# Optimization experiments

Measured on AMD Instinct MI355X. Metric: run time of the kernel, lower is better.

## Reference

```python
import jax, jax.numpy as jnp
import numpy as np

B, T, C, H = 4, 2048, 1024, 16
D = C // H  # head dim = 64

def setup_inputs() -> dict:
    key = jax.random.key(0)
    k1, k2, k3 = jax.random.split(key, 3)
    y = jax.random.normal(k1, (B, T, C), dtype=jnp.float32)
    W_attn = jax.random.normal(k2, (C, 3 * C), dtype=jnp.float32) * (1.0 / np.sqrt(C))
    b_attn = jnp.zeros((3 * C,), dtype=jnp.float32)
    W_proj = jax.random.normal(k3, (C, C), dtype=jnp.float32) * (1.0 / np.sqrt(C))
    b_proj = jnp.zeros((C,), dtype=jnp.float32)
    return {"y": y, "W_attn": W_attn, "b_attn": b_attn, "W_proj": W_proj, "b_proj": b_proj}

def reference(y, W_attn, b_attn, W_proj, b_proj):
    # qkv projection: [B,T,C] @ [C,3C] -> split into q,k,v
    qkv = y @ W_attn + b_attn
    q, k, v = jnp.split(qkv, 3, axis=-1)
    # [B,T,C] -> [B,H,T,D]
    q = q.reshape(B, T, H, D).swapaxes(1, 2)
    k = k.reshape(B, T, H, D).swapaxes(1, 2)
    v = v.reshape(B, T, H, D).swapaxes(1, 2)
    # scaled dot-product attention, non-causal (config default), dropout=0
    att = jnp.einsum('bhtd,bhrd->bhtr', q, k) * (1.0 / jnp.sqrt(jnp.float32(D)))
    att = jax.nn.softmax(att, axis=-1)
    out = jnp.einsum('bhts,bhsd->bhtd', att, v)
    out = out.swapaxes(1, 2).reshape(B, T, C)
    return out @ W_proj + b_proj
```

## Files before the change

kernel.cpp:

```cpp
#include <hip/hip_runtime.h>
#include <hip/hip_bf16.h>
#include <stdint.h>

#define B_ 4
#define T_ 2048
#define C_ 1024
#define H_ 16
#define D_ 64

typedef short bf16x8 __attribute__((ext_vector_type(8)));
typedef float f32x4 __attribute__((ext_vector_type(4)));
typedef unsigned short u16;

#define QSCALE 0.18033688011112042f

__device__ __forceinline__ u16 f2bf(float f) {
    __hip_bfloat16 h = __float2bfloat16(f);
    return *reinterpret_cast<u16*>(&h);
}

__device__ __forceinline__ float fexp2(float x) {
    float r;
    asm("v_exp_f32 %0, %1" : "=v"(r) : "v"(x));
    return r;
}

__device__ __forceinline__ void gload16(const void* g, void* l) {
    __builtin_amdgcn_global_load_lds(
        (const __attribute__((address_space(1))) unsigned int*)g,
        (__attribute__((address_space(3))) unsigned int*)l, 16, 0, 0);
}

__global__ void k_cast_bf16(const float* __restrict__ src, u16* __restrict__ dst, int n) {
    int i = (blockIdx.x * blockDim.x + threadIdx.x) * 4;
    if (i >= n) return;
    float4 f = *reinterpret_cast<const float4*>(src + i);
    ushort4 o;
    o.x = f2bf(f.x); o.y = f2bf(f.y); o.z = f2bf(f.z); o.w = f2bf(f.w);
    *reinterpret_cast<ushort4*>(dst + i) = o;
}

__global__ void k_transpose_bf16(const float* __restrict__ src, u16* __restrict__ dst,
                                 int R, int Cc) {
    __shared__ float tile[32][33];
    int c0 = blockIdx.x * 32, r0 = blockIdx.y * 32;
    int tx = threadIdx.x, ty = threadIdx.y;
#pragma unroll
    for (int i = 0; i < 4; i++)
        tile[ty + i * 8][tx] = src[(size_t)(r0 + ty + i * 8) * Cc + c0 + tx];
    __syncthreads();
#pragma unroll
    for (int i = 0; i < 4; i++)
        dst[(size_t)(c0 + ty + i * 8) * R + r0 + tx] = f2bf(tile[tx][ty + i * 8]);
}

template <int EPI>
__launch_bounds__(256, 2)
__global__ void k_gemm(const u16* __restrict__ A, const u16* __restrict__ Bt,
                       const float* __restrict__ bias, int K, int N,
                       float* __restrict__ outf,
                       u16* __restrict__ qw, u16* __restrict__ kw, u16* __restrict__ vw) {
    __shared__ u16 As[128 * 64];
    __shared__ u16 Bs[128 * 64];
    const int tid = threadIdx.x;
    const int lane = tid & 63, w = tid >> 6;
    const int m0 = blockIdx.x * 128, n0 = blockIdx.y * 128;
    const int wm = (w >> 1) * 64, wn = (w & 1) * 64;
    const int lr = lane & 15, lg = lane >> 4;

    f32x4 acc[4][4];
#pragma unroll
    for (int i = 0; i < 4; i++)
#pragma unroll
        for (int j = 0; j < 4; j++) acc[i][j] = (f32x4){0.f, 0.f, 0.f, 0.f};

    const int nk = K >> 6;
    for (int kt = 0; kt < nk; ++kt) {
        const int k0 = kt * 64;
#pragma unroll
        for (int i = 0; i < 4; i++) {
            int c = i * 256 + tid;
            int row = c >> 3, k8 = (c & 7) << 3;
            gload16(A + (size_t)(m0 + row) * K + k0 + k8, (char*)As + i * 4096 + w * 1024);
            gload16(Bt + (size_t)(n0 + row) * K + k0 + k8, (char*)Bs + i * 4096 + w * 1024);
        }
        __syncthreads();
#pragma unroll
        for (int kk = 0; kk < 2; ++kk) {
            bf16x8 af[4], bfr[4];
#pragma unroll
            for (int mf = 0; mf < 4; ++mf)
                af[mf] = *reinterpret_cast<const bf16x8*>(&As[(wm + mf * 16 + lr) * 64 + kk * 32 + lg * 8]);
#pragma unroll
            for (int nf = 0; nf < 4; ++nf)
                bfr[nf] = *reinterpret_cast<const bf16x8*>(&Bs[(wn + nf * 16 + lr) * 64 + kk * 32 + lg * 8]);
#pragma unroll
            for (int mf = 0; mf < 4; ++mf)
#pragma unroll
                for (int nf = 0; nf < 4; ++nf)
                    acc[mf][nf] = __builtin_amdgcn_mfma_f32_16x16x32_bf16(af[mf], bfr[nf], acc[mf][nf], 0, 0, 0);
        }
        __syncthreads();
    }

    if (EPI == 0) {
#pragma unroll
        for (int mf = 0; mf < 4; ++mf)
#pragma unroll
            for (int nf = 0; nf < 4; ++nf) {
                int ng = n0 + wn + nf * 16 + lr;
                float bs = bias[ng];
#pragma unroll
                for (int r = 0; r < 4; ++r) {
                    int mg = m0 + wm + mf * 16 + lg * 4 + r;
                    outf[(size_t)mg * N + ng] = acc[mf][nf][r] + bs;
                }
            }
    } else {
        const int sec = n0 >> 10;
        const float sc = (sec == 0) ? QSCALE : 1.0f;
#pragma unroll
        for (int mf = 0; mf < 4; ++mf)
#pragma unroll
            for (int nf = 0; nf < 4; ++nf) {
                int ng = n0 + wn + nf * 16 + lr;
                float bs = bias[ng];
                int hd = ng & 1023;
                int h = hd >> 6, d = hd & 63;
                int mgb = m0 + wm + mf * 16 + lg * 4;
                int b = mgb >> 11, t0v = mgb & 2047;
                if (sec == 2) {
                    ushort4 pk;
                    pk.x = f2bf(acc[mf][nf][0] + bs);
                    pk.y = f2bf(acc[mf][nf][1] + bs);
                    pk.z = f2bf(acc[mf][nf][2] + bs);
                    pk.w = f2bf(acc[mf][nf][3] + bs);
                    *reinterpret_cast<ushort4*>(&vw[((size_t)(b * H_ + h) * D_ + d) * T_ + t0v]) = pk;
                } else {
                    u16* dst = (sec == 0) ? qw : kw;
#pragma unroll
                    for (int r = 0; r < 4; ++r)
                        dst[((size_t)(b * H_ + h) * T_ + t0v + r) * D_ + d] = f2bf((acc[mf][nf][r] + bs) * sc);
                }
            }
    }
}

__launch_bounds__(256, 4)
__global__ void k_attn(const u16* __restrict__ qw, const u16* __restrict__ kw,
                       const u16* __restrict__ vw, u16* __restrict__ attn) {
    __shared__ u16 Ks[2][64][64];
    __shared__ u16 Vs[2][64][64];
    const int tid = threadIdx.x, lane = tid & 63, w = tid >> 6;
    const int lr = lane & 15, lg = lane >> 4;
    const int bid = blockIdx.x;
    const int logical = (bid & 7) * 128 + (bid >> 3);
    const int bh = logical >> 4, qb = logical & 15;
    const int b = bh >> 4, h = bh & 15;
    const int q0 = qb * 128 + w * 32;
    const u16* qbase = qw + (size_t)bh * T_ * D_;
    const u16* kbase = kw + (size_t)bh * T_ * D_;
    const u16* vbase = vw + (size_t)bh * D_ * T_;

    bf16x8 qf[2][2];
#pragma unroll
    for (int jq = 0; jq < 2; jq++)
#pragma unroll
        for (int kd = 0; kd < 2; kd++)
            qf[jq][kd] = *reinterpret_cast<const bf16x8*>(
                &qbase[(size_t)(q0 + jq * 16 + lr) * D_ + kd * 32 + lg * 8]);

    auto stageK = [&](int kt, int buf) {
#pragma unroll
        for (int i = 0; i < 2; i++) {
            int idx = i * 256 + tid;
            int row = idx >> 3, ch = idx & 7;
            int gch = ch ^ ((row & 3) | (((row >> 3) & 1) << 2));
            gload16(kbase + ((size_t)(kt * 64 + row) * 64 + gch * 8),
                    (char*)&Ks[buf][0][0] + i * 4096 + w * 1024);
        }
    };
    auto stageV = [&](int kt, int buf) {
#pragma unroll
        for (int i = 0; i < 2; i++) {
            int idx = i * 256 + tid;
            int row = idx >> 3, ch = idx & 7;
            int gch = ch ^ (row & 7);
            gload16(vbase + ((size_t)row * T_ + kt * 64 + gch * 8),
                    (char*)&Vs[buf][0][0] + i * 4096 + w * 1024);
        }
    };

    f32x4 o[4][2];
#pragma unroll
    for (int md = 0; md < 4; md++)
#pragma unroll
        for (int jq = 0; jq < 2; jq++) o[md][jq] = (f32x4){0.f, 0.f, 0.f, 0.f};
    float l_run[2] = {0.f, 0.f};

    const int karow_base = ((lr >> 2) << 3) + (lr & 3);
    const int skl = ((lr & 3) | (((lr >> 2) & 1) << 2)) << 4;

    const int NT = T_ / 64;
    stageK(0, 0);
    stageV(0, 0);

    for (int kt = 0; kt < NT; ++kt) {
        const int cur = kt & 1;
        if (kt + 1 < NT) {
            stageK(kt + 1, cur ^ 1);
            stageV(kt + 1, cur ^ 1);
            asm volatile("s_waitcnt vmcnt(4)" ::: "memory");
        } else {
            asm volatile("s_waitcnt vmcnt(0)" ::: "memory");
        }
        __builtin_amdgcn_s_barrier();

        bf16x8 pfrag[2][2];
#pragma unroll
        for (int g = 0; g < 2; g++) {
            f32x4 st[2][2];
#pragma unroll
            for (int t = 0; t < 2; t++)
#pragma unroll
                for (int jq = 0; jq < 2; jq++) st[t][jq] = (f32x4){0.f, 0.f, 0.f, 0.f};
            __builtin_amdgcn_s_setprio(1);
#pragma unroll
            for (int t = 0; t < 2; t++) {
                int row = g * 32 + karow_base + t * 4;
#pragma unroll
                for (int kd = 0; kd < 2; kd++) {
                    bf16x8 ka = *reinterpret_cast<const bf16x8*>(
                        (const char*)&Ks[cur][0][0] + row * 128 + ((kd * 64 + lg * 16) ^ skl));
#pragma unroll
                    for (int jq = 0; jq < 2; jq++)
                        st[t][jq] = __builtin_amdgcn_mfma_f32_16x16x32_bf16(ka, qf[jq][kd], st[t][jq], 0, 0, 0);
                }
            }
            __builtin_amdgcn_s_setprio(0);
#pragma unroll
            for (int jq = 0; jq < 2; jq++) {
                float p0 = fexp2(st[0][jq][0]), p1 = fexp2(st[0][jq][1]);
                float p2 = fexp2(st[0][jq][2]), p3 = fexp2(st[0][jq][3]);
                float p4 = fexp2(st[1][jq][0]), p5 = fexp2(st[1][jq][1]);
                float p6 = fexp2(st[1][jq][2]), p7 = fexp2(st[1][jq][3]);
                l_run[jq] += ((p0 + p1) + (p2 + p3)) + ((p4 + p5) + (p6 + p7));
                pfrag[jq][g] = (bf16x8){(short)f2bf(p0), (short)f2bf(p1),
                                        (short)f2bf(p2), (short)f2bf(p3),
                                        (short)f2bf(p4), (short)f2bf(p5),
                                        (short)f2bf(p6), (short)f2bf(p7)};
            }
        }

#pragma unroll
        for (int g = 0; g < 2; g++) {
            bf16x8 va[4];
#pragma unroll
            for (int md = 0; md < 4; md++) {
                int row = md * 16 + lr;
                va[md] = *reinterpret_cast<const bf16x8*>(
                    (const char*)&Vs[cur][0][0] + row * 128 + ((g * 64 + lg * 16) ^ ((row & 7) << 4)));
            }
            __builtin_amdgcn_s_setprio(1);
#pragma unroll
            for (int md = 0; md < 4; md++)
#pragma unroll
                for (int jq = 0; jq < 2; jq++)
                    o[md][jq] = __builtin_amdgcn_mfma_f32_16x16x32_bf16(va[md], pfrag[jq][g], o[md][jq], 0, 0, 0);
            __builtin_amdgcn_s_setprio(0);
        }

        __builtin_amdgcn_s_barrier();
    }

#pragma unroll
    for (int jq = 0; jq < 2; jq++) {
        float l = l_run[jq];
        l += __shfl_xor(l, 16);
        l += __shfl_xor(l, 32);
        float rinv = 1.f / l;
        int q = q0 + jq * 16 + lr;
#pragma unroll
        for (int md = 0; md < 4; md++) {
            int d0 = md * 16 + lg * 4;
            ushort4 pk;
            pk.x = f2bf(o[md][jq][0] * rinv);
            pk.y = f2bf(o[md][jq][1] * rinv);
            pk.z = f2bf(o[md][jq][2] * rinv);
            pk.w = f2bf(o[md][jq][3] * rinv);
            *reinterpret_cast<ushort4*>(&attn[((size_t)(b * T_ + q)) * C_ + h * D_ + d0]) = pk;
        }
    }
}

extern "C" void kernel_launch(void* const* d_in, const int* in_sizes, int n_in,
                              void* d_out, int out_size, void* d_ws, size_t ws_size,
                              hipStream_t stream) {
    const float* y = (const float*)d_in[0];
    const float* W_attn = (const float*)d_in[1];
    const float* b_attn = (const float*)d_in[2];
    const float* W_proj = (const float*)d_in[3];
    const float* b_proj = (const float*)d_in[4];

    char* ws = (char*)d_ws;
    u16* y_bf = (u16*)(ws);
    u16* WaT  = (u16*)(ws + 16777216);
    u16* WpT  = (u16*)(ws + 16777216 + 6291456);
    u16* q_ws = (u16*)(ws + 25165824);
    u16* k_ws = (u16*)(ws + 25165824 + 16777216);
    u16* v_ws = (u16*)(ws + 25165824 + 33554432);
    u16* attn = (u16*)(ws + 25165824 + 50331648);

    k_cast_bf16<<<8192, 256, 0, stream>>>(y, y_bf, B_ * T_ * C_);
    k_transpose_bf16<<<dim3(96, 32), dim3(32, 8), 0, stream>>>(W_attn, WaT, 1024, 3072);
    k_transpose_bf16<<<dim3(32, 32), dim3(32, 8), 0, stream>>>(W_proj, WpT, 1024, 1024);
    k_gemm<1><<<dim3(64, 24), 256, 0, stream>>>(y_bf, WaT, b_attn, 1024, 3072,
                                                nullptr, q_ws, k_ws, v_ws);
    k_attn<<<1024, 256, 0, stream>>>(q_ws, k_ws, v_ws, attn);
    k_gemm<0><<<dim3(64, 8), 256, 0, stream>>>(attn, WpT, b_proj, 1024, 1024,
                                               (float*)d_out, nullptr, nullptr, nullptr);
}
```

Baseline: 200.1 us.

## Fuse prep kernels into one launch and widen attention waves to 64 queries

The three preprocessing kernels (cast of y, transpose of W_attn, transpose of W_proj) are merged into one launch that dispatches on block index, which removes two launch gaps. The attention kernel now uses 2 waves per block instead of 4, and each wave handles 64 query rows instead of 32. Each K/V fragment read from LDS therefore feeds twice as many MFMAs, while the number of staging loads per thread doubles. In exchange, accumulator and register pressure rises and fewer waves per block are available to hide latency.

Measured after the change: 188.8 us. -5.7%, faster.

```diff
diff --git a/kernel.cpp b/kernel.cpp
--- a/kernel.cpp
+++ b/kernel.cpp
@@ -31,20 +31,31 @@
         (__attribute__((address_space(3))) unsigned int*)l, 16, 0, 0);
 }
 
-__global__ void k_cast_bf16(const float* __restrict__ src, u16* __restrict__ dst, int n) {
-    int i = (blockIdx.x * blockDim.x + threadIdx.x) * 4;
-    if (i >= n) return;
-    float4 f = *reinterpret_cast<const float4*>(src + i);
-    ushort4 o;
-    o.x = f2bf(f.x); o.y = f2bf(f.y); o.z = f2bf(f.z); o.w = f2bf(f.w);
-    *reinterpret_cast<ushort4*>(dst + i) = o;
-}
-
-__global__ void k_transpose_bf16(const float* __restrict__ src, u16* __restrict__ dst,
-                                 int R, int Cc) {
+__global__ void k_prep(const float* __restrict__ y, u16* __restrict__ y_bf,
+                       const float* __restrict__ Wa, u16* __restrict__ WaT,
+                       const float* __restrict__ Wp, u16* __restrict__ WpT) {
+    const int bid = blockIdx.x, tid = threadIdx.x;
+    if (bid < 8192) {
+        int i = (bid * 256 + tid) * 4;
+        float4 f = *reinterpret_cast<const float4*>(y + i);
+        ushort4 o;
+        o.x = f2bf(f.x); o.y = f2bf(f.y); o.z = f2bf(f.z); o.w = f2bf(f.w);
+        *reinterpret_cast<ushort4*>(y_bf + i) = o;
+        return;
+    }
     __shared__ float tile[32][33];
-    int c0 = blockIdx.x * 32, r0 = blockIdx.y * 32;
-    int tx = threadIdx.x, ty = threadIdx.y;
+    const float* src; u16* dst; int R, Cc, bx, by;
+    if (bid < 8192 + 3072) {
+        int idx = bid - 8192;
+        src = Wa; dst = WaT; R = 1024; Cc = 3072;
+        bx = idx % 96; by = idx / 96;
+    } else {
+        int idx = bid - 11264;
+        src = Wp; dst = WpT; R = 1024; Cc = 1024;
+        bx = idx & 31; by = idx >> 5;
+    }
+    int c0 = bx * 32, r0 = by * 32;
+    int tx = tid & 31, ty = tid >> 5;
 #pragma unroll
     for (int i = 0; i < 4; i++)
         tile[ty + i * 8][tx] = src[(size_t)(r0 + ty + i * 8) * Cc + c0 + tx];
@@ -146,7 +157,7 @@
     }
 }
 
-__launch_bounds__(256, 4)
+__launch_bounds__(128, 2)
 __global__ void k_attn(const u16* __restrict__ qw, const u16* __restrict__ kw,
                        const u16* __restrict__ vw, u16* __restrict__ attn) {
     __shared__ u16 Ks[2][64][64];
@@ -157,14 +168,14 @@
     const int logical = (bid & 7) * 128 + (bid >> 3);
     const int bh = logical >> 4, qb = logical & 15;
     const int b = bh >> 4, h = bh & 15;
-    const int q0 = qb * 128 + w * 32;
+    const int q0 = qb * 128 + w * 64;
     const u16* qbase = qw + (size_t)bh * T_ * D_;
     const u16* kbase = kw + (size_t)bh * T_ * D_;
     const u16* vbase = vw + (size_t)bh * D_ * T_;
 
-    bf16x8 qf[2][2];
-#pragma unroll
-    for (int jq = 0; jq < 2; jq++)
+    bf16x8 qf[4][2];
+#pragma unroll
+    for (int jq = 0; jq < 4; jq++)
 #pragma unroll
         for (int kd = 0; kd < 2; kd++)
             qf[jq][kd] = *reinterpret_cast<const bf16x8*>(
@@ -172,31 +183,31 @@
 
     auto stageK = [&](int kt, int buf) {
 #pragma unroll
-        for (int i = 0; i < 2; i++) {
-            int idx = i * 256 + tid;
+        for (int i = 0; i < 4; i++) {
+            int idx = i * 128 + tid;
             int row = idx >> 3, ch = idx & 7;
             int gch = ch ^ ((row & 3) | (((row >> 3) & 1) << 2));
             gload16(kbase + ((size_t)(kt * 64 + row) * 64 + gch * 8),
-                    (char*)&Ks[buf][0][0] + i * 4096 + w * 1024);
+                    (char*)&Ks[buf][0][0] + i * 2048 + w * 1024);
         }
     };
     auto stageV = [&](int kt, int buf) {
 #pragma unroll
-        for (int i = 0; i < 2; i++) {
-            int idx = i * 256 + tid;
+        for (int i = 0; i < 4; i++) {
+            int idx = i * 128 + tid;
             int row = idx >> 3, ch = idx & 7;
             int gch = ch ^ (row & 7);
             gload16(vbase + ((size_t)row * T_ + kt * 64 + gch * 8),
-                    (char*)&Vs[buf][0][0] + i * 4096 + w * 1024);
+                    (char*)&Vs[buf][0][0] + i * 2048 + w * 1024);
         }
     };
 
-    f32x4 o[4][2];
+    f32x4 o[4][4];
 #pragma unroll
     for (int md = 0; md < 4; md++)
 #pragma unroll
-        for (int jq = 0; jq < 2; jq++) o[md][jq] = (f32x4){0.f, 0.f, 0.f, 0.f};
-    float l_run[2] = {0.f, 0.f};
+        for (int jq = 0; jq < 4; jq++) o[md][jq] = (f32x4){0.f, 0.f, 0.f, 0.f};
+    float l_run[4] = {0.f, 0.f, 0.f, 0.f};
 
     const int karow_base = ((lr >> 2) << 3) + (lr & 3);
     const int skl = ((lr & 3) | (((lr >> 2) & 1) << 2)) << 4;
@@ -210,20 +221,20 @@
         if (kt + 1 < NT) {
             stageK(kt + 1, cur ^ 1);
             stageV(kt + 1, cur ^ 1);
-            asm volatile("s_waitcnt vmcnt(4)" ::: "memory");
+            asm volatile("s_waitcnt vmcnt(8)" ::: "memory");
         } else {
             asm volatile("s_waitcnt vmcnt(0)" ::: "memory");
         }
         __builtin_amdgcn_s_barrier();
 
-        bf16x8 pfrag[2][2];
+        bf16x8 pfrag[4][2];
 #pragma unroll
         for (int g = 0; g < 2; g++) {
-            f32x4 st[2][2];
+            f32x4 st[2][4];
 #pragma unroll
             for (int t = 0; t < 2; t++)
 #pragma unroll
-                for (int jq = 0; jq < 2; jq++) st[t][jq] = (f32x4){0.f, 0.f, 0.f, 0.f};
+                for (int jq = 0; jq < 4; jq++) st[t][jq] = (f32x4){0.f, 0.f, 0.f, 0.f};
             __builtin_amdgcn_s_setprio(1);
 #pragma unroll
             for (int t = 0; t < 2; t++) {
@@ -233,13 +244,13 @@
                     bf16x8 ka = *reinterpret_cast<const bf16x8*>(
                         (const char*)&Ks[cur][0][0] + row * 128 + ((kd * 64 + lg * 16) ^ skl));
 #pragma unroll
-                    for (int jq = 0; jq < 2; jq++)
+                    for (int jq = 0; jq < 4; jq++)
                         st[t][jq] = __builtin_amdgcn_mfma_f32_16x16x32_bf16(ka, qf[jq][kd], st[t][jq], 0, 0, 0);
                 }
             }
             __builtin_amdgcn_s_setprio(0);
 #pragma unroll
-            for (int jq = 0; jq < 2; jq++) {
+            for (int jq = 0; jq < 4; jq++) {
                 float p0 = fexp2(st[0][jq][0]), p1 = fexp2(st[0][jq][1]);
                 float p2 = fexp2(st[0][jq][2]), p3 = fexp2(st[0][jq][3]);
                 float p4 = fexp2(st[1][jq][0]), p5 = fexp2(st[1][jq][1]);
@@ -265,7 +276,7 @@
 #pragma unroll
             for (int md = 0; md < 4; md++)
 #pragma unroll
-                for (int jq = 0; jq < 2; jq++)
+                for (int jq = 0; jq < 4; jq++)
                     o[md][jq] = __builtin_amdgcn_mfma_f32_16x16x32_bf16(va[md], pfrag[jq][g], o[md][jq], 0, 0, 0);
             __builtin_amdgcn_s_setprio(0);
         }
@@ -274,7 +285,7 @@
     }
 
 #pragma unroll
-    for (int jq = 0; jq < 2; jq++) {
+    for (int jq = 0; jq < 4; jq++) {
         float l = l_run[jq];
         l += __shfl_xor(l, 16);
         l += __shfl_xor(l, 32);
@@ -311,12 +322,10 @@
     u16* v_ws = (u16*)(ws + 25165824 + 33554432);
     u16* attn = (u16*)(ws + 25165824 + 50331648);
 
-    k_cast_bf16<<<8192, 256, 0, stream>>>(y, y_bf, B_ * T_ * C_);
-    k_transpose_bf16<<<dim3(96, 32), dim3(32, 8), 0, stream>>>(W_attn, WaT, 1024, 3072);
-    k_transpose_bf16<<<dim3(32, 32), dim3(32, 8), 0, stream>>>(W_proj, WpT, 1024, 1024);
+    k_prep<<<12288, 256, 0, stream>>>(y, y_bf, W_attn, WaT, W_proj, WpT);
     k_gemm<1><<<dim3(64, 24), 256, 0, stream>>>(y_bf, WaT, b_attn, 1024, 3072,
                                                 nullptr, q_ws, k_ws, v_ws);
-    k_attn<<<1024, 256, 0, stream>>>(q_ws, k_ws, v_ws, attn);
+    k_attn<<<1024, 128, 0, stream>>>(q_ws, k_ws, v_ws, attn);
     k_gemm<0><<<dim3(64, 8), 256, 0, stream>>>(attn, WpT, b_proj, 1024, 1024,
                                                (float*)d_out, nullptr, nullptr, nullptr);
 }
```
